# Optimization experiments

Hardware: AMD Instinct MI355X
Metric: run time of the kernel (lower is better)

The kernel has to match this reference:

```python
import jax, jax.numpy as jnp
import numpy as np

DN = ('NCHW', 'OIHW', 'NCHW')


def conv2d(x, w, b):
    y = jax.lax.conv_general_dilated(x, w, (1, 1), 'SAME', dimension_numbers=DN)
    return y + b[None, :, None, None]


def dyn_filter(x, Wa, ba, Wb, bb, Wc, bc):
    # KPN-style head: predict 81 per-pixel 9x9 filter taps, softmax-normalized.
    h = jax.nn.relu(conv2d(x, Wa, ba))
    h = jax.nn.relu(conv2d(h, Wb, bb))
    f = conv2d(h, Wc, bc)            # (N, 81, H, W)
    return jax.nn.softmax(f, axis=1)


def apply_dynamic_conv(x, f):
    # Equivalent to pad(4) + unfold(9x9) + mul + sum, without materializing
    # the (N,81,H,W)*... patch tensor: accumulate 81 shifted slices.
    N, C, H, W = x.shape  # C == 1
    xp = jnp.pad(x, ((0, 0), (0, 0), (4, 4), (4, 4)))
    out = jnp.zeros((N, 1, H, W), x.dtype)
    for dy in range(9):
        for dx in range(9):
            k = dy * 9 + dx  # matches unfold(2).unfold(3).permute(0,1,4,5,2,3) tap order
            out = out + xp[:, :, dy:dy + H, dx:dx + W] * f[:, k:k + 1]
    return out


def nearest_resize(x, oh, ow):
    _, _, ih, iw = x.shape
    ri = jnp.arange(oh) * ih // oh   # matches torch F.interpolate mode='nearest'
    rj = jnp.arange(ow) * iw // ow
    return x[:, :, ri][:, :, :, rj]


def setup_inputs() -> dict:
    key = jax.random.key(0)
    ks = jax.random.split(key, 8)
    s = 0.05
    return {
        'x': jax.random.normal(ks[0], (2, 1, 512, 512), jnp.float32),
        'g': jax.random.normal(ks[1], (2, 1, 512, 512), jnp.float32),
        'fWa': jax.random.normal(ks[2], (5, 64, 1, 3, 3), jnp.float32) * s,
        'fba': jnp.zeros((5, 64), jnp.float32),
        'fWb': jax.random.normal(ks[3], (5, 64, 64, 3, 3), jnp.float32) * s,
        'fbb': jnp.zeros((5, 64), jnp.float32),
        'fWc': jax.random.normal(ks[4], (5, 81, 64, 3, 3), jnp.float32) * s,
        'fbc': jnp.zeros((5, 81), jnp.float32),
        'W2a': jax.random.normal(ks[5], (64, 5, 3, 3), jnp.float32) * s,
        'b2a': jnp.zeros((64,), jnp.float32),
        'W2b': jax.random.normal(ks[6], (1, 64, 3, 3), jnp.float32) * s,
        'b2b': jnp.zeros((1,), jnp.float32),
    }


def reference(x, g, fWa, fba, fWb, fbb, fWc, fbc, W2a, b2a, W2b, b2b):
    N, C, h, w = x.shape
    scales = [
        x,
        nearest_resize(x, h // 2, w // 2),
        nearest_resize(x, h // 4, w // 4),
        nearest_resize(x, h // 8, w // 8),
        g,
    ]
    outs = []
    for i, s in enumerate(scales):
        f = dyn_filter(s, fWa[i], fba[i], fWb[i], fbb[i], fWc[i], fbc[i])
        y = apply_dynamic_conv(s, f)
        if y.shape[2] != h or y.shape[3] != w:
            y = nearest_resize(y, h, w)
        outs.append(y)
    cat = jnp.concatenate(outs, axis=1)  # (N, 5, h, w)
    hid = jax.nn.relu(conv2d(cat, W2a, b2a))
    return conv2d(hid, W2b, b2b)
```

## Files before the change

### kernel.cpp

```cpp
#include <hip/hip_runtime.h>
#include <math.h>

typedef _Float16 half8 __attribute__((ext_vector_type(8)));
typedef _Float16 half4v __attribute__((ext_vector_type(4)));
typedef float f32x4 __attribute__((ext_vector_type(4)));

#define LOG2E 1.44269504f

__device__ __forceinline__ void pack_generic(int rem, int NT, int COUT, float scale,
                                             const float* __restrict__ src,
                                             _Float16* __restrict__ dst) {
  int j = rem & 7, lane = (rem >> 3) & 63, rest = rem >> 9;
  int t = rest % NT, s = rest / NT;
  int oc = t * 16 + (lane & 15);
  int tap = s >> 1;
  int ic = (s & 1) * 32 + ((lane >> 4) & 3) * 8 + j;
  float v = (oc < COUT) ? src[((size_t)oc * 64 + ic) * 9 + tap] * scale : 0.f;
  dst[rem] = (_Float16)v;
}

__global__ void prep_all_kernel(const float* __restrict__ fWa, const float* __restrict__ fWb,
                                const float* __restrict__ fWc, const float* __restrict__ W2a,
                                const float* __restrict__ W2b, const float* __restrict__ x,
                                _Float16* __restrict__ Bp1, _Float16* __restrict__ BpA,
                                _Float16* __restrict__ BpB, _Float16* __restrict__ Bpb,
                                _Float16* __restrict__ Bpc,
                                _Float16* __restrict__ s1, _Float16* __restrict__ s2,
                                _Float16* __restrict__ s3) {
  int idx = blockIdx.x * blockDim.x + threadIdx.x;
  if (idx < 184320) {
    int sc = idx / 36864, rem = idx - sc * 36864;
    pack_generic(rem, 4, 64, 1.f, fWb + sc * 36864, Bpb + sc * 36864);
  } else if (idx < 460800) {
    int i2 = idx - 184320;
    int sc = i2 / 55296, rem = i2 - sc * 55296;
    pack_generic(rem, 6, 81, LOG2E, fWc + sc * 46656, Bpc + sc * 55296);
  } else if (idx < 471040) {
    int i2 = idx - 460800;
    int sc = i2 >> 11, rem = i2 & 2047;
    int j = rem & 7, lane = (rem >> 3) & 63, nt = rem >> 9;
    int oc = nt * 16 + (lane & 15);
    int k = ((lane >> 4) & 3) * 8 + j;
    float v = (k < 9) ? fWa[sc * 576 + oc * 9 + k] : 0.f;
    Bp1[sc * 2048 + rem] = (_Float16)v;
  } else if (idx < 475136) {
    int rem = idx - 471040;
    int j = rem & 7, lane = (rem >> 3) & 63;
    int nt = (rem >> 9) & 3, s = rem >> 11;
    int oc = nt * 16 + (lane & 15);
    int k = s * 32 + ((lane >> 4) & 3) * 8 + j;
    float v = 0.f;
    if (k < 45) { int ic = k / 9, tap = k - ic * 9; v = W2a[(oc * 5 + ic) * 9 + tap]; }
    BpA[rem] = (_Float16)v;
  } else if (idx < 484352) {
    pack_generic(idx - 475136, 1, 1, 1.f, W2b, BpB);
  } else if (idx < 615424) {
    int i2 = idx - 484352;
    int n = i2 >> 16, p = i2 & 65535, rr = p >> 8, cc = p & 255;
    s1[i2] = (_Float16)x[(size_t)n * 262144 + (size_t)(rr * 2) * 512 + cc * 2];
  } else if (idx < 648192) {
    int i2 = idx - 615424;
    int n = i2 >> 14, p = i2 & 16383, rr = p >> 7, cc = p & 127;
    s2[i2] = (_Float16)x[(size_t)n * 262144 + (size_t)(rr * 4) * 512 + cc * 4];
  } else if (idx < 656384) {
    int i2 = idx - 648192;
    int n = i2 >> 12, p = i2 & 4095, rr = p >> 6, cc = p & 63;
    s3[i2] = (_Float16)x[(size_t)n * 262144 + (size_t)(rr * 8) * 512 + cc * 8];
  }
}

__device__ __forceinline__ int xcd_swizzle(int bid) {
  return (bid & 7) * 596 + (bid >> 3);
}

__device__ __forceinline__ void map_block(int bid, int& sc, int& n, int& bx, int& by,
                                          int& Hs, int& RS, int& h2off) {
  if (bid < 2048) { sc = 0; Hs = 512; RS = 1; h2off = 0;
    int t = bid; n = t >> 10; t &= 1023; by = t >> 5; bx = t & 31; }
  else if (bid < 4096) { sc = 4; Hs = 512; RS = 1; h2off = 33554432;
    int t = bid - 2048; n = t >> 10; t &= 1023; by = t >> 5; bx = t & 31; }
  else if (bid < 4608) { sc = 1; Hs = 256; RS = 2; h2off = 67108864;
    int t = bid - 4096; n = t >> 8; t &= 255; by = t >> 4; bx = t & 15; }
  else if (bid < 4736) { sc = 2; Hs = 128; RS = 4; h2off = 75497472;
    int t = bid - 4608; n = t >> 6; t &= 63; by = t >> 3; bx = t & 7; }
  else { sc = 3; Hs = 64; RS = 8; h2off = 77594624;
    int t = bid - 4736; n = t >> 4; t &= 15; by = t >> 2; bx = t & 3; }
}

__device__ __forceinline__ const void* pick_src(int sc, const float* x, const float* g,
                                                const _Float16* s1, const _Float16* s2,
                                                const _Float16* s3, int& sStr, bool& f16s) {
  if (sc == 0) { sStr = 262144; f16s = false; return x; }
  if (sc == 1) { sStr = 65536; f16s = true; return s1; }
  if (sc == 2) { sStr = 16384; f16s = true; return s2; }
  if (sc == 3) { sStr = 4096; f16s = true; return s3; }
  sStr = 262144; f16s = false; return g;
}

__device__ __forceinline__ float src_load(const void* p, bool f16s, size_t off) {
  return f16s ? (float)((const _Float16*)p)[off] : ((const float*)p)[off];
}

template <int MT, int NT, bool SWAP, int NTHR>
__device__ __forceinline__ void mfma_acc18(const _Float16* slab, const half8* __restrict__ Bp,
                                           half8* __restrict__ Bs,
                                           f32x4 (&acc)[MT][NT], int tid) {
  const int lane = tid & 63;
  const int wv = tid >> 6;
  const int quad = lane >> 4;
  const int ln15 = lane & 15;
  const f32x4 zz = {0.f, 0.f, 0.f, 0.f};
#pragma unroll
  for (int mt = 0; mt < MT; ++mt)
#pragma unroll
    for (int nt = 0; nt < NT; ++nt) acc[mt][nt] = zz;
  auto step = [&](int s, half8 (&bf)[NT]) {
    const int tap = s >> 1;
    const int dy = tap / 3;
    const int dx = tap - dy * 3;
    const int C = dx + ln15;
    const int qsw = (((s & 1) * 4 + quad) ^ (C & 7));
    const _Float16* base = slab + C * 64 + qsw * 8;
    half8 af[MT];
#pragma unroll
    for (int mt = 0; mt < MT; ++mt)
      af[mt] = *(const half8*)(base + (wv * MT + mt + dy) * (18 * 64));
#pragma unroll
    for (int mt = 0; mt < MT; ++mt)
#pragma unroll
      for (int nt = 0; nt < NT; ++nt)
        acc[mt][nt] = SWAP
          ? __builtin_amdgcn_mfma_f32_16x16x32_f16(bf[nt], af[mt], acc[mt][nt], 0, 0, 0)
          : __builtin_amdgcn_mfma_f32_16x16x32_f16(af[mt], bf[nt], acc[mt][nt], 0, 0, 0);
  };
  constexpr int CH = 2 * NT * 64;
  for (int i = tid; i < CH; i += NTHR) Bs[i] = Bp[i];
  __syncthreads();
#pragma unroll 1
  for (int c = 0; c < 9; ++c) {
    const int buf = c & 1;
    if (c < 8) {
      const half8* gsrc = Bp + (2 * (c + 1)) * (NT * 64);
      half8* dst = Bs + (buf ^ 1) * CH;
      for (int i = tid; i < CH; i += NTHR) dst[i] = gsrc[i];
    }
    half8 bf[NT];
#pragma unroll
    for (int nt = 0; nt < NT; ++nt) bf[nt] = Bs[buf * CH + nt * 64 + lane];
    step(2 * c, bf);
#pragma unroll
    for (int nt = 0; nt < NT; ++nt) bf[nt] = Bs[buf * CH + NT * 64 + nt * 64 + lane];
    step(2 * c + 1, bf);
    __syncthreads();
  }
}

template <int MT, int NT, int COUT, int COUTP, bool RELU, typename OutT, int NTHR>
__device__ __forceinline__ void mfma_body(const _Float16* slab, const half8* __restrict__ Bp,
                                          half8* __restrict__ Bs,
                                          const float* __restrict__ bias,
                                          OutT* __restrict__ out,
                                          int H, int W, int gr0, int gc0, int tid) {
  f32x4 acc[MT][NT];
  mfma_acc18<MT, NT, false, NTHR>(slab, Bp, Bs, acc, tid);
  const int lane = tid & 63;
  const int wv = tid >> 6;
  const int quad = lane >> 4;
  const int ln15 = lane & 15;
  float bvv[NT];
#pragma unroll
  for (int nt = 0; nt < NT; ++nt) {
    const int oc = nt * 16 + ln15;
    bvv[nt] = (oc < COUT) ? bias[oc] : 0.f;
  }
#pragma unroll
  for (int mt = 0; mt < MT; ++mt) {
    const int gr = gr0 + wv * MT + mt;
#pragma unroll
    for (int reg = 0; reg < 4; ++reg) {
      const int gc = gc0 + quad * 4 + reg;
#pragma unroll
      for (int nt = 0; nt < NT; ++nt) {
        const int oc = nt * 16 + ln15;
        float v = acc[mt][nt][reg] + bvv[nt];
        if (RELU) v = fmaxf(v, 0.f);
        if (oc < COUTP) out[((size_t)gr * W + gc) * COUTP + oc] = (OutT)v;
      }
    }
  }
}

__global__ __launch_bounds__(512, 4)
void conv12_ms_kernel(const float* __restrict__ x, const float* __restrict__ g,
                      const _Float16* __restrict__ s1, const _Float16* __restrict__ s2,
                      const _Float16* __restrict__ s3,
                      const half8* __restrict__ Bp1b, const float* __restrict__ fba,
                      const half8* __restrict__ Bpbb, const float* __restrict__ fbb,
                      _Float16* __restrict__ h2) {
  __shared__ float xs[20 * 20];
  __shared__ __align__(16) _Float16 slab[18 * 18 * 64];
  __shared__ half8 BsS[2 * 2 * 4 * 64];
  int sc, n, bx, by, Hs, RS, h2off;
  map_block(xcd_swizzle(blockIdx.x), sc, n, bx, by, Hs, RS, h2off);
  int sStr; bool f16s;
  const void* src = pick_src(sc, x, g, s1, s2, s3, sStr, f16s);
  _Float16* out = h2 + h2off + (size_t)n * Hs * Hs * 64;
  const half8* Bp1 = Bp1b + sc * 256;
  const half8* Bp = Bpbb + sc * 4608;
  const float* ba = fba + sc * 64;
  const float* bb = fbb + sc * 64;
  const int H = Hs, W = Hs;
  const int tid = threadIdx.x;
  const int gr0 = by * 16, gc0 = bx * 16;
  for (int i = tid; i < 400; i += 512) {
    int R = i / 20, C = i % 20;
    int gr = gr0 - 2 + R, gc = gc0 - 2 + C;
    xs[i] = (gr >= 0 && gr < H && gc >= 0 && gc < W)
                ? src_load(src, f16s, (size_t)n * sStr + (size_t)gr * W + gc) : 0.f;
  }
  __syncthreads();
  const int lane = tid & 63;
  const int wv = tid >> 6;
  const int quad = lane >> 4;
  const int ln15 = lane & 15;
  half8 bf1[4];
  float b1v[4][4];
#pragma unroll
  for (int nt = 0; nt < 4; ++nt) {
    bf1[nt] = Bp1[nt * 64 + lane];
#pragma unroll
    for (int reg = 0; reg < 4; ++reg) b1v[nt][reg] = ba[nt * 16 + quad * 4 + reg];
  }
  int off1[8];
  bool v1[8];
#pragma unroll
  for (int j = 0; j < 8; ++j) {
    int k = quad * 8 + j;
    v1[j] = (k < 9);
    off1[j] = v1[j] ? ((k / 3) * 20 + (k % 3)) : 0;
  }
  const f32x4 zz = {0.f, 0.f, 0.f, 0.f};
#pragma unroll 1
  for (int mt = wv; mt < 21; mt += 8) {
    int p = mt * 16 + ln15;
    int pcl = (p < 323) ? p : 323;
    int Rg = pcl / 18, Cg = pcl - Rg * 18;
    int base = Rg * 20 + Cg;
    half8 af;
#pragma unroll
    for (int j = 0; j < 8; ++j)
      af[j] = v1[j] ? (_Float16)xs[base + off1[j]] : (_Float16)0.f;
    f32x4 a1[4] = {zz, zz, zz, zz};
#pragma unroll
    for (int nt = 0; nt < 4; ++nt)
      a1[nt] = __builtin_amdgcn_mfma_f32_16x16x32_f16(bf1[nt], af, a1[nt], 0, 0, 0);
    if (p < 324) {
      int R2 = p / 18, C2 = p - R2 * 18;
      int gr = gr0 - 1 + R2, gc = gc0 - 1 + C2;
      bool inb = (gr >= 0 && gr < H && gc >= 0 && gc < W);
      _Float16* sb = slab + p * 64 + (quad & 1) * 4;
      const int csw = C2 & 7;
#pragma unroll
      for (int nt = 0; nt < 4; ++nt) {
        half4v w;
#pragma unroll
        for (int reg = 0; reg < 4; ++reg) {
          float v = inb ? fmaxf(a1[nt][reg] + b1v[nt][reg], 0.f) : 0.f;
          w[reg] = (_Float16)v;
        }
        const int chunk = nt * 2 + (quad >> 1);
        *(half4v*)(sb + ((chunk ^ csw) * 8)) = w;
      }
    }
  }
  __syncthreads();
  mfma_body<2, 4, 64, 64, true, _Float16, 512>(slab, Bp, BsS, bb, out, H, W, gr0, gc0, tid);
}

__global__ __launch_bounds__(512, 4)
void conv3sd_ms_kernel(const _Float16* __restrict__ h2, const half8* __restrict__ Bpcb,
                       const float* __restrict__ fbc,
                       const float* __restrict__ x, const float* __restrict__ g,
                       const _Float16* __restrict__ s1, const _Float16* __restrict__ s2,
                       const _Float16* __restrict__ s3, float* __restrict__ cat) {
  constexpr int MT = 2;
  __shared__ __align__(16) _Float16 slab[324 * 40];
  __shared__ float xs[24 * 24];
  __shared__ half8 BsS[2 * 768];
  int sc, n, bx, by, Hs, RS, h2off;
  map_block(xcd_swizzle(blockIdx.x), sc, n, bx, by, Hs, RS, h2off);
  int sStr; bool f16s;
  const void* src = pick_src(sc, x, g, s1, s2, s3, sStr, f16s);
  const _Float16* in = h2 + h2off + (size_t)n * Hs * Hs * 64;
  const half8* Bp = Bpcb + sc * 6912;
  const float* bias = fbc + sc * 81;
  float* catp = cat + (size_t)(sc * 2 + n) * 262144;
  const int H = Hs, W = Hs;
  const int tid = threadIdx.x;
  const int gr0 = by * 16, gc0 = bx * 16;
  const int lane = tid & 63;
  const int wv = tid >> 6;
  const int quad = lane >> 4;
  const int ln15 = lane & 15;
  for (int i = tid; i < 576; i += 512) {
    int R = i / 24, C = i % 24;
    int gr = gr0 - 4 + R, gc = gc0 - 4 + C;
    xs[i] = (gr >= 0 && gr < H && gc >= 0 && gc < W)
                ? src_load(src, f16s, (size_t)n * sStr + (size_t)gr * W + gc) : 0.f;
  }
  auto stage_load = [&](int h, half8 (&stg)[3], int (&soff)[3], bool (&sok)[3]) {
#pragma unroll
    for (int it = 0; it < 3; ++it) {
      int i = tid + it * 512;
      bool ok = (i < 1296);
      int chunk = i & 3, px = i >> 2;
      int R = px / 18, C = px - R * 18;
      int gr = gr0 - 1 + R, gc = gc0 - 1 + C;
      half8 v = {0, 0, 0, 0, 0, 0, 0, 0};
      if (ok && gr >= 0 && gr < H && gc >= 0 && gc < W)
        v = *(const half8*)(in + ((size_t)gr * W + gc) * 64 + (h * 4 + chunk) * 8);
      stg[it] = v;
      soff[it] = px * 40 + chunk * 8;
      sok[it] = ok;
    }
  };
  auto stage_write = [&](half8 (&stg)[3], int (&soff)[3], bool (&sok)[3]) {
#pragma unroll
    for (int it = 0; it < 3; ++it)
      if (sok[it]) *(half8*)(slab + soff[it]) = stg[it];
  };
  auto stageB2 = [&](int t0, int t1, int h, int buf) {
    half8* dst = BsS + buf * 768;
    const half8* g0 = Bp + (size_t)(t0 * 2 + h) * 384;
    const half8* g1 = Bp + (size_t)(t1 * 2 + h) * 384;
#pragma unroll
    for (int it = 0; it < 2; ++it) {
      int i = tid + it * 512;
      if (i < 768) dst[i] = (i < 384) ? g0[i] : g1[i - 384];
    }
  };
  auto stageB1 = [&](int h, int buf) {
    half8* dst = BsS + buf * 768;
    const half8* g0 = Bp + (size_t)(16 + h) * 384;
    if (tid < 384) dst[tid] = g0[tid];
  };

  f32x4 acc[MT][6];
  const f32x4 zz = {0.f, 0.f, 0.f, 0.f};
#pragma unroll
  for (int mt = 0; mt < MT; ++mt)
#pragma unroll
    for (int nt = 0; nt < 6; ++nt) acc[mt][nt] = zz;

  auto ctap = [&](int tap, half8 (&bf)[6]) {
    const int dy = tap / 3;
    const int dx = tap - dy * 3;
    const int C = dx + ln15;
    const _Float16* base = slab + C * 40 + quad * 8;
    half8 af[MT];
#pragma unroll
    for (int mt = 0; mt < MT; ++mt)
      af[mt] = *(const half8*)(base + (wv * MT + mt + dy) * 720);
#pragma unroll
    for (int mt = 0; mt < MT; ++mt)
#pragma unroll
      for (int nt = 0; nt < 6; ++nt)
        acc[mt][nt] = __builtin_amdgcn_mfma_f32_16x16x32_f16(bf[nt], af[mt], acc[mt][nt], 0, 0, 0);
  };
  auto run_taps = [&](int h, int b0) {
#pragma unroll 1
    for (int c = 0; c < 4; ++c) {
      const int buf = b0 ^ (c & 1);
      if (c < 3) stageB2(2 * c + 2, 2 * c + 3, h, buf ^ 1);
      else       stageB1(h, buf ^ 1);
      half8 bf[6];
#pragma unroll
      for (int nt = 0; nt < 6; ++nt) bf[nt] = BsS[buf * 768 + nt * 64 + lane];
      ctap(2 * c, bf);
#pragma unroll
      for (int nt = 0; nt < 6; ++nt) bf[nt] = BsS[buf * 768 + 384 + nt * 64 + lane];
      ctap(2 * c + 1, bf);
      __syncthreads();
    }
    const int buf = b0;
    half8 bf[6];
#pragma unroll
    for (int nt = 0; nt < 6; ++nt) bf[nt] = BsS[buf * 768 + nt * 64 + lane];
    ctap(8, bf);
  };

  half8 stgA[3]; int soffA[3]; bool sokA[3];
  half8 stgB[3]; int soffB[3]; bool sokB[3];
  stage_load(0, stgA, soffA, sokA);
  stage_write(stgA, soffA, sokA);
  stageB2(0, 1, 0, 0);
  __syncthreads();
  stage_load(1, stgB, soffB, sokB);
  run_taps(0, 0);
  __syncthreads();
  stage_write(stgB, soffB, sokB);
  stageB2(0, 1, 1, 0);
  __syncthreads();
  run_taps(1, 0);

  float bvv[6][4];
  int dyx[6][4];
  bool vv[6][4];
#pragma unroll
  for (int nt = 0; nt < 6; ++nt)
#pragma unroll
    for (int reg = 0; reg < 4; ++reg) {
      int ch = nt * 16 + quad * 4 + reg;
      bool ok = (ch < 81);
      vv[nt][reg] = ok;
      bvv[nt][reg] = ok ? bias[ch] * LOG2E : 0.f;
      int dy = ch / 9, dx = ch - dy * 9;
      dyx[nt][reg] = ok ? dy * 24 + dx : 0;
    }
  const int lrs = (RS == 2) ? 1 : ((RS == 4) ? 2 : 3);
#pragma unroll
  for (int mt = 0; mt < MT; ++mt) {
    const float* xb = xs + (wv * MT + mt) * 24 + ln15;
    float sum = 0.f, y = 0.f;
#pragma unroll
    for (int nt = 0; nt < 6; ++nt)
#pragma unroll
      for (int reg = 0; reg < 4; ++reg) {
        if (vv[nt][reg]) {
          float e = exp2f(acc[mt][nt][reg] + bvv[nt][reg]);
          sum += e;
          y = fmaf(e, xb[dyx[nt][reg]], y);
        }
      }
    sum += __shfl_xor(sum, 16, 64);
    sum += __shfl_xor(sum, 32, 64);
    y += __shfl_xor(y, 16, 64);
    y += __shfl_xor(y, 32, 64);
    const float o = y / sum;
    const int gr = gr0 + wv * MT + mt, gc = gc0 + ln15;
    if (RS == 1) {
      if (quad == 0) catp[(size_t)gr * 512 + gc] = o;
    } else {
      for (int t = quad; t < RS * RS; t += 4) {
        int a = t >> lrs, b = t & (RS - 1);
        catp[((size_t)(gr * RS + a)) * 512 + (gc * RS + b)] = o;
      }
    }
  }
}

__global__ __launch_bounds__(512, 4)
void tail_fused_kernel(const float* __restrict__ cat,
                       const half8* __restrict__ BpA, const float* __restrict__ b2a,
                       const half8* __restrict__ BpB, const float* __restrict__ b2b,
                       float* __restrict__ out) {
  __shared__ float cs[20 * 20 * 5];
  __shared__ __align__(16) _Float16 hid[18 * 18 * 64];
  __shared__ half8 BsS[2 * 2 * 1 * 64];
  const int n = blockIdx.z;
  float* op = out + (size_t)n * (512 * 512);
  const int tid = threadIdx.x;
  const int gr0 = blockIdx.y * 16, gc0 = blockIdx.x * 16;
  for (int i = tid; i < 2000; i += 512) {
    int ic = i / 400, px = i - ic * 400;
    int R = px / 20, C = px - R * 20;
    int gr = gr0 - 2 + R, gc = gc0 - 2 + C;
    cs[px * 5 + ic] = (gr >= 0 && gr < 512 && gc >= 0 && gc < 512)
                ? cat[(size_t)(ic * 2 + n) * 262144 + (size_t)gr * 512 + gc] : 0.f;
  }
  __syncthreads();
  const int lane = tid & 63;
  const int wv = tid >> 6;
  const int quad = lane >> 4;
  const int ln15 = lane & 15;
  int goff[2][8];
  bool gok[2][8];
#pragma unroll
  for (int s = 0; s < 2; ++s)
#pragma unroll
    for (int j = 0; j < 8; ++j) {
      int k = s * 32 + quad * 8 + j;
      bool ok = (k < 45);
      int ic = k / 9;
      int tap = k - ic * 9;
      int dy = tap / 3, dx = tap - dy * 3;
      goff[s][j] = ok ? ((dy * 20 + dx) * 5 + ic) : 0;
      gok[s][j] = ok;
    }
  half8 bfA[2][4];
  float bAv[4][4];
#pragma unroll
  for (int s = 0; s < 2; ++s)
#pragma unroll
    for (int nt = 0; nt < 4; ++nt) bfA[s][nt] = BpA[(s * 4 + nt) * 64 + lane];
#pragma unroll
  for (int nt = 0; nt < 4; ++nt)
#pragma unroll
    for (int reg = 0; reg < 4; ++reg) bAv[nt][reg] = b2a[nt * 16 + quad * 4 + reg];
  const f32x4 zz = {0.f, 0.f, 0.f, 0.f};
#pragma unroll 1
  for (int mt = wv; mt < 21; mt += 8) {
    int p = mt * 16 + ln15;
    int pcl = (p < 323) ? p : 323;
    int base = (pcl / 18) * 100 + (pcl % 18) * 5;
    f32x4 acc1[4] = {zz, zz, zz, zz};
#pragma unroll
    for (int s = 0; s < 2; ++s) {
      half8 af;
#pragma unroll
      for (int j = 0; j < 8; ++j) {
        float a = gok[s][j] ? cs[base + goff[s][j]] : 0.f;
        af[j] = (_Float16)a;
      }
#pragma unroll
      for (int nt = 0; nt < 4; ++nt)
        acc1[nt] = __builtin_amdgcn_mfma_f32_16x16x32_f16(bfA[s][nt], af, acc1[nt], 0, 0, 0);
    }
    if (p < 324) {
      int R2 = p / 18, C2 = p - R2 * 18;
      int gr = gr0 - 1 + R2, gc = gc0 - 1 + C2;
      bool inb = (gr >= 0 && gr < 512 && gc >= 0 && gc < 512);
      _Float16* sb = hid + p * 64 + (quad & 1) * 4;
      const int csw = C2 & 7;
#pragma unroll
      for (int nt = 0; nt < 4; ++nt) {
        half4v w;
#pragma unroll
        for (int reg = 0; reg < 4; ++reg) {
          float v = inb ? fmaxf(acc1[nt][reg] + bAv[nt][reg], 0.f) : 0.f;
          w[reg] = (_Float16)v;
        }
        const int chunk = nt * 2 + (quad >> 1);
        *(half4v*)(sb + ((chunk ^ csw) * 8)) = w;
      }
    }
  }
  __syncthreads();
  mfma_body<2, 1, 1, 1, false, float, 512>(hid, BpB, BsS, b2b, op, 512, 512, gr0, gc0, tid);
}

extern "C" void kernel_launch(void* const* d_in, const int* in_sizes, int n_in,
                              void* d_out, int out_size, void* d_ws, size_t ws_size,
                              hipStream_t stream) {
  (void)in_sizes; (void)n_in; (void)out_size; (void)ws_size;
  const float* x   = (const float*)d_in[0];
  const float* g   = (const float*)d_in[1];
  const float* fWa = (const float*)d_in[2];
  const float* fba = (const float*)d_in[3];
  const float* fWb = (const float*)d_in[4];
  const float* fbb = (const float*)d_in[5];
  const float* fWc = (const float*)d_in[6];
  const float* fbc = (const float*)d_in[7];
  const float* W2a = (const float*)d_in[8];
  const float* b2a = (const float*)d_in[9];
  const float* W2b = (const float*)d_in[10];
  const float* b2b = (const float*)d_in[11];
  float* out = (float*)d_out;
  float* ws = (float*)d_ws;

  float* Bp1F = ws;
  float* BpAF = Bp1F + 5120;
  float* BpBF = BpAF + 2048;
  float* BpbF = BpBF + 4608;
  float* BpcF = BpbF + 92160;
  float* s1F  = BpcF + 138240;
  float* s2F  = s1F + 65536;
  float* s3F  = s2F + 16384;
  float* cat  = s3F + 4096;
  float* h2F  = cat + 2621440;
  _Float16* s1 = (_Float16*)s1F;
  _Float16* s2 = (_Float16*)s2F;
  _Float16* s3 = (_Float16*)s3F;
  _Float16* h2 = (_Float16*)h2F;
  const half8* Bp1 = (const half8*)Bp1F;
  const half8* BpA = (const half8*)BpAF;
  const half8* BpB = (const half8*)BpBF;
  const half8* Bpb = (const half8*)BpbF;
  const half8* Bpc = (const half8*)BpcF;

  prep_all_kernel<<<2564, 256, 0, stream>>>(fWa, fWb, fWc, W2a, W2b, x,
                                            (_Float16*)Bp1F, (_Float16*)BpAF,
                                            (_Float16*)BpBF, (_Float16*)BpbF,
                                            (_Float16*)BpcF, s1, s2, s3);
  conv12_ms_kernel<<<4768, 512, 0, stream>>>(x, g, s1, s2, s3, Bp1, fba, Bpb, fbb, h2);
  conv3sd_ms_kernel<<<4768, 512, 0, stream>>>(h2, Bpc, fbc, x, g, s1, s2, s3, cat);
  tail_fused_kernel<<<dim3(32, 32, 2), 512, 0, stream>>>(cat, BpA, b2a, BpB, b2b, out);
}
```

Baseline: 377.4 us.

## Enlarge conv3 tile to 32x16 pixels and drop register-staged slab prefetch

The fused conv3/softmax/dynamic-conv kernel now gives each block a 32x16 output tile (MT=4) instead of 16x16, halving the grid and adding new block-mapping and XCD swizzle helpers. This amortizes the per-block weight staging and the halo loads over more pixels. The register-staged prefetch of the second input half is replaced with direct global-to-LDS staging after the first half's compute. The trade-off is more LDS and registers per block, launch bounds lowered to 2 blocks per SM, and less overlap of loads with MFMA work.

After: 427.7 us. +13.3%, slower.

```diff
diff --git a/kernel.cpp b/kernel.cpp
--- a/kernel.cpp
+++ b/kernel.cpp
@@ -87,6 +87,24 @@
     int t = bid - 4736; n = t >> 4; t &= 15; by = t >> 2; bx = t & 3; }
 }
 
+__device__ __forceinline__ int xcd_swizzle32(int bid) {
+  return (bid & 7) * 298 + (bid >> 3);
+}
+
+__device__ __forceinline__ void map_block32(int bid, int& sc, int& n, int& bx, int& by,
+                                            int& Hs, int& RS, int& h2off) {
+  if (bid < 1024) { sc = 0; Hs = 512; RS = 1; h2off = 0;
+    int t = bid; n = t >> 9; t &= 511; by = t >> 5; bx = t & 31; }
+  else if (bid < 2048) { sc = 4; Hs = 512; RS = 1; h2off = 33554432;
+    int t = bid - 1024; n = t >> 9; t &= 511; by = t >> 5; bx = t & 31; }
+  else if (bid < 2304) { sc = 1; Hs = 256; RS = 2; h2off = 67108864;
+    int t = bid - 2048; n = t >> 7; t &= 127; by = t >> 4; bx = t & 15; }
+  else if (bid < 2368) { sc = 2; Hs = 128; RS = 4; h2off = 75497472;
+    int t = bid - 2304; n = t >> 5; t &= 31; by = t >> 3; bx = t & 7; }
+  else { sc = 3; Hs = 64; RS = 8; h2off = 77594624;
+    int t = bid - 2368; n = t >> 3; t &= 7; by = t >> 2; bx = t & 3; }
+}
+
 __device__ __forceinline__ const void* pick_src(int sc, const float* x, const float* g,
                                                 const _Float16* s1, const _Float16* s2,
                                                 const _Float16* s3, int& sStr, bool& f16s) {
@@ -277,18 +295,18 @@
   mfma_body<2, 4, 64, 64, true, _Float16, 512>(slab, Bp, BsS, bb, out, H, W, gr0, gc0, tid);
 }
 
-__global__ __launch_bounds__(512, 4)
+__global__ __launch_bounds__(512, 2)
 void conv3sd_ms_kernel(const _Float16* __restrict__ h2, const half8* __restrict__ Bpcb,
                        const float* __restrict__ fbc,
                        const float* __restrict__ x, const float* __restrict__ g,
                        const _Float16* __restrict__ s1, const _Float16* __restrict__ s2,
                        const _Float16* __restrict__ s3, float* __restrict__ cat) {
-  constexpr int MT = 2;
-  __shared__ __align__(16) _Float16 slab[324 * 40];
-  __shared__ float xs[24 * 24];
+  constexpr int MT = 4;
+  __shared__ __align__(16) _Float16 slab[612 * 40];
+  __shared__ float xs[40 * 24];
   __shared__ half8 BsS[2 * 768];
   int sc, n, bx, by, Hs, RS, h2off;
-  map_block(xcd_swizzle(blockIdx.x), sc, n, bx, by, Hs, RS, h2off);
+  map_block32(xcd_swizzle32(blockIdx.x), sc, n, bx, by, Hs, RS, h2off);
   int sStr; bool f16s;
   const void* src = pick_src(sc, x, g, s1, s2, s3, sStr, f16s);
   const _Float16* in = h2 + h2off + (size_t)n * Hs * Hs * 64;
@@ -297,37 +315,28 @@
   float* catp = cat + (size_t)(sc * 2 + n) * 262144;
   const int H = Hs, W = Hs;
   const int tid = threadIdx.x;
-  const int gr0 = by * 16, gc0 = bx * 16;
+  const int gr0 = by * 32, gc0 = bx * 16;
   const int lane = tid & 63;
   const int wv = tid >> 6;
   const int quad = lane >> 4;
   const int ln15 = lane & 15;
-  for (int i = tid; i < 576; i += 512) {
+  for (int i = tid; i < 960; i += 512) {
     int R = i / 24, C = i % 24;
     int gr = gr0 - 4 + R, gc = gc0 - 4 + C;
     xs[i] = (gr >= 0 && gr < H && gc >= 0 && gc < W)
                 ? src_load(src, f16s, (size_t)n * sStr + (size_t)gr * W + gc) : 0.f;
   }
-  auto stage_load = [&](int h, half8 (&stg)[3], int (&soff)[3], bool (&sok)[3]) {
-#pragma unroll
-    for (int it = 0; it < 3; ++it) {
-      int i = tid + it * 512;
-      bool ok = (i < 1296);
+  auto stage_slab = [&](int h) {
+#pragma unroll 1
+    for (int i = tid; i < 2448; i += 512) {
       int chunk = i & 3, px = i >> 2;
       int R = px / 18, C = px - R * 18;
       int gr = gr0 - 1 + R, gc = gc0 - 1 + C;
       half8 v = {0, 0, 0, 0, 0, 0, 0, 0};
-      if (ok && gr >= 0 && gr < H && gc >= 0 && gc < W)
+      if (gr >= 0 && gr < H && gc >= 0 && gc < W)
         v = *(const half8*)(in + ((size_t)gr * W + gc) * 64 + (h * 4 + chunk) * 8);
-      stg[it] = v;
-      soff[it] = px * 40 + chunk * 8;
-      sok[it] = ok;
-    }
-  };
-  auto stage_write = [&](half8 (&stg)[3], int (&soff)[3], bool (&sok)[3]) {
-#pragma unroll
-    for (int it = 0; it < 3; ++it)
-      if (sok[it]) *(half8*)(slab + soff[it]) = stg[it];
+      *(half8*)(slab + px * 40 + chunk * 8) = v;
+    }
   };
   auto stageB2 = [&](int t0, int t1, int h, int buf) {
     half8* dst = BsS + buf * 768;
@@ -389,16 +398,12 @@
     ctap(8, bf);
   };
 
-  half8 stgA[3]; int soffA[3]; bool sokA[3];
-  half8 stgB[3]; int soffB[3]; bool sokB[3];
-  stage_load(0, stgA, soffA, sokA);
-  stage_write(stgA, soffA, sokA);
+  stage_slab(0);
   stageB2(0, 1, 0, 0);
   __syncthreads();
-  stage_load(1, stgB, soffB, sokB);
   run_taps(0, 0);
   __syncthreads();
-  stage_write(stgB, soffB, sokB);
+  stage_slab(1);
   stageB2(0, 1, 1, 0);
   __syncthreads();
   run_taps(1, 0);
@@ -583,6 +588,6 @@
                                             (_Float16*)BpBF, (_Float16*)BpbF,
                                             (_Float16*)BpcF, s1, s2, s3);
   conv12_ms_kernel<<<4768, 512, 0, stream>>>(x, g, s1, s2, s3, Bp1, fba, Bpb, fbb, h2);
-  conv3sd_ms_kernel<<<4768, 512, 0, stream>>>(h2, Bpc, fbc, x, g, s1, s2, s3, cat);
+  conv3sd_ms_kernel<<<2384, 512, 0, stream>>>(h2, Bpc, fbc, x, g, s1, s2, s3, cat);
   tail_fused_kernel<<<dim3(32, 32, 2), 512, 0, stream>>>(cat, BpA, b2a, BpB, b2b, out);
 }
```

## Load conv3 input slab and weights via global_load_lds with XOR swizzle

Applied to the files above, without the earlier changes.

Restructures the final 64->81 conv stage. The full 64-channel halo slab now goes into LDS in a single pass, using direct global-to-LDS loads for interior tiles and an XOR-swizzled layout, instead of two 32-channel halves staged through registers. Weights are double-buffered per tap using 4-byte direct-to-LDS loads with vmcnt/barrier pipelining, and s_setprio is raised around the MFMA blocks. The larger LDS footprint lowers the occupancy target from 4 to 2 blocks per CU.

New measurement: 383.9 us. About the same (+1.7%).

```diff
diff --git a/kernel.cpp b/kernel.cpp
--- a/kernel.cpp
+++ b/kernel.cpp
@@ -6,6 +6,16 @@
 typedef float f32x4 __attribute__((ext_vector_type(4)));
 
 #define LOG2E 1.44269504f
+
+typedef __attribute__((address_space(1))) const unsigned int gas_u32;
+typedef __attribute__((address_space(3))) unsigned int las_u32;
+
+__device__ __forceinline__ void gll16(const void* gsrc, void* ldst) {
+  __builtin_amdgcn_global_load_lds((gas_u32*)gsrc, (las_u32*)ldst, 16, 0, 0);
+}
+__device__ __forceinline__ void gll4(const void* gsrc, void* ldst) {
+  __builtin_amdgcn_global_load_lds((gas_u32*)gsrc, (las_u32*)ldst, 4, 0, 0);
+}
 
 __device__ __forceinline__ void pack_generic(int rem, int NT, int COUT, float scale,
                                              const float* __restrict__ src,
@@ -277,16 +287,15 @@
   mfma_body<2, 4, 64, 64, true, _Float16, 512>(slab, Bp, BsS, bb, out, H, W, gr0, gc0, tid);
 }
 
-__global__ __launch_bounds__(512, 4)
+__global__ __launch_bounds__(512, 2)
 void conv3sd_ms_kernel(const _Float16* __restrict__ h2, const half8* __restrict__ Bpcb,
                        const float* __restrict__ fbc,
                        const float* __restrict__ x, const float* __restrict__ g,
                        const _Float16* __restrict__ s1, const _Float16* __restrict__ s2,
                        const _Float16* __restrict__ s3, float* __restrict__ cat) {
-  constexpr int MT = 2;
-  __shared__ __align__(16) _Float16 slab[324 * 40];
+  __shared__ __align__(16) _Float16 slab[384 * 64];
+  __shared__ __align__(16) _Float16 Bsd[2][6144];
   __shared__ float xs[24 * 24];
-  __shared__ half8 BsS[2 * 768];
   int sc, n, bx, by, Hs, RS, h2off;
   map_block(xcd_swizzle(blockIdx.x), sc, n, bx, by, Hs, RS, h2off);
   int sStr; bool f16s;
@@ -302,106 +311,100 @@
   const int wv = tid >> 6;
   const int quad = lane >> 4;
   const int ln15 = lane & 15;
+
   for (int i = tid; i < 576; i += 512) {
     int R = i / 24, C = i % 24;
     int gr = gr0 - 4 + R, gc = gc0 - 4 + C;
     xs[i] = (gr >= 0 && gr < H && gc >= 0 && gc < W)
                 ? src_load(src, f16s, (size_t)n * sStr + (size_t)gr * W + gc) : 0.f;
   }
-  auto stage_load = [&](int h, half8 (&stg)[3], int (&soff)[3], bool (&sok)[3]) {
-#pragma unroll
-    for (int it = 0; it < 3; ++it) {
-      int i = tid + it * 512;
-      bool ok = (i < 1296);
-      int chunk = i & 3, px = i >> 2;
+
+  const bool interior = (gr0 > 0) && (gc0 > 0) && (gr0 + 17 <= H) && (gc0 + 17 <= W);
+  if (interior) {
+    const int pxb0 = wv * 48;
+#pragma unroll
+    for (int k = 0; k < 6; ++k) {
+      const int pxb = pxb0 + k * 8;
+      int px = pxb + (lane >> 3);
+      int pcl = (px < 324) ? px : 323;
+      int R = pcl / 18, C = pcl - R * 18;
+      int l = (lane & 7) ^ (C & 7);
+      gll16((const char*)(in + ((size_t)(gr0 - 1 + R) * W + (gc0 - 1 + C)) * 64 + l * 8),
+            (char*)slab + (size_t)pxb * 128);
+    }
+  } else {
+    for (int i = tid; i < 2592; i += 512) {
+      int px = i >> 3, pslot = i & 7;
       int R = px / 18, C = px - R * 18;
       int gr = gr0 - 1 + R, gc = gc0 - 1 + C;
+      int l = pslot ^ (C & 7);
       half8 v = {0, 0, 0, 0, 0, 0, 0, 0};
-      if (ok && gr >= 0 && gr < H && gc >= 0 && gc < W)
-        v = *(const half8*)(in + ((size_t)gr * W + gc) * 64 + (h * 4 + chunk) * 8);
-      stg[it] = v;
-      soff[it] = px * 40 + chunk * 8;
-      sok[it] = ok;
-    }
+      if (gr >= 0 && gr < H && gc >= 0 && gc < W)
+        v = *(const half8*)(in + ((size_t)gr * W + gc) * 64 + l * 8);
+      *(half8*)(slab + (size_t)px * 64 + pslot * 8) = v;
+    }
+  }
+
+  auto stageB = [&](int t, int buf) {
+    const char* s = (const char*)(Bp + (size_t)t * 768) + wv * 1536 + lane * 4;
+    char* d = (char*)(&Bsd[buf][0]) + wv * 1536;
+#pragma unroll
+    for (int i = 0; i < 6; ++i) gll4(s + i * 256, d + i * 256);
   };
-  auto stage_write = [&](half8 (&stg)[3], int (&soff)[3], bool (&sok)[3]) {
-#pragma unroll
-    for (int it = 0; it < 3; ++it)
-      if (sok[it]) *(half8*)(slab + soff[it]) = stg[it];
+  stageB(0, 0);
+  stageB(1, 1);
+  asm volatile("s_waitcnt lgkmcnt(0)" ::: "memory");
+
+  f32x4 acc[2][6];
+  const f32x4 zz = {0.f, 0.f, 0.f, 0.f};
+#pragma unroll
+  for (int mt = 0; mt < 2; ++mt)
+#pragma unroll
+    for (int nt = 0; nt < 6; ++nt) acc[mt][nt] = zz;
+
+  auto tap_body = [&](int t, int buf) {
+    const int dy = t / 3, dx = t - dy * 3;
+    const int C = dx + ln15;
+    const int cx = C & 7;
+    const _Float16* bb = &Bsd[buf][0];
+#pragma unroll
+    for (int h = 0; h < 2; ++h) {
+      half8 bf[6];
+#pragma unroll
+      for (int nt = 0; nt < 6; ++nt)
+        bf[nt] = *(const half8*)(bb + h * 3072 + (nt * 64 + lane) * 8);
+      half8 af[2];
+#pragma unroll
+      for (int mt = 0; mt < 2; ++mt) {
+        const int px = (wv * 2 + mt + dy) * 18 + C;
+        af[mt] = *(const half8*)(slab + (size_t)px * 64 + ((h * 4 + quad) ^ cx) * 8);
+      }
+      __builtin_amdgcn_s_setprio(1);
+#pragma unroll
+      for (int mt = 0; mt < 2; ++mt)
+#pragma unroll
+        for (int nt = 0; nt < 6; ++nt)
+          acc[mt][nt] =
+              __builtin_amdgcn_mfma_f32_16x16x32_f16(bf[nt], af[mt], acc[mt][nt], 0, 0, 0);
+      __builtin_amdgcn_s_setprio(0);
+    }
   };
-  auto stageB2 = [&](int t0, int t1, int h, int buf) {
-    half8* dst = BsS + buf * 768;
-    const half8* g0 = Bp + (size_t)(t0 * 2 + h) * 384;
-    const half8* g1 = Bp + (size_t)(t1 * 2 + h) * 384;
-#pragma unroll
-    for (int it = 0; it < 2; ++it) {
-      int i = tid + it * 512;
-      if (i < 768) dst[i] = (i < 384) ? g0[i] : g1[i - 384];
-    }
-  };
-  auto stageB1 = [&](int h, int buf) {
-    half8* dst = BsS + buf * 768;
-    const half8* g0 = Bp + (size_t)(16 + h) * 384;
-    if (tid < 384) dst[tid] = g0[tid];
-  };
-
-  f32x4 acc[MT][6];
-  const f32x4 zz = {0.f, 0.f, 0.f, 0.f};
-#pragma unroll
-  for (int mt = 0; mt < MT; ++mt)
-#pragma unroll
-    for (int nt = 0; nt < 6; ++nt) acc[mt][nt] = zz;
-
-  auto ctap = [&](int tap, half8 (&bf)[6]) {
-    const int dy = tap / 3;
-    const int dx = tap - dy * 3;
-    const int C = dx + ln15;
-    const _Float16* base = slab + C * 40 + quad * 8;
-    half8 af[MT];
-#pragma unroll
-    for (int mt = 0; mt < MT; ++mt)
-      af[mt] = *(const half8*)(base + (wv * MT + mt + dy) * 720);
-#pragma unroll
-    for (int mt = 0; mt < MT; ++mt)
-#pragma unroll
-      for (int nt = 0; nt < 6; ++nt)
-        acc[mt][nt] = __builtin_amdgcn_mfma_f32_16x16x32_f16(bf[nt], af[mt], acc[mt][nt], 0, 0, 0);
-  };
-  auto run_taps = [&](int h, int b0) {
+
 #pragma unroll 1
-    for (int c = 0; c < 4; ++c) {
-      const int buf = b0 ^ (c & 1);
-      if (c < 3) stageB2(2 * c + 2, 2 * c + 3, h, buf ^ 1);
-      else       stageB1(h, buf ^ 1);
-      half8 bf[6];
-#pragma unroll
-      for (int nt = 0; nt < 6; ++nt) bf[nt] = BsS[buf * 768 + nt * 64 + lane];
-      ctap(2 * c, bf);
-#pragma unroll
-      for (int nt = 0; nt < 6; ++nt) bf[nt] = BsS[buf * 768 + 384 + nt * 64 + lane];
-      ctap(2 * c + 1, bf);
-      __syncthreads();
-    }
-    const int buf = b0;
-    half8 bf[6];
-#pragma unroll
-    for (int nt = 0; nt < 6; ++nt) bf[nt] = BsS[buf * 768 + nt * 64 + lane];
-    ctap(8, bf);
-  };
-
-  half8 stgA[3]; int soffA[3]; bool sokA[3];
-  half8 stgB[3]; int soffB[3]; bool sokB[3];
-  stage_load(0, stgA, soffA, sokA);
-  stage_write(stgA, soffA, sokA);
-  stageB2(0, 1, 0, 0);
-  __syncthreads();
-  stage_load(1, stgB, soffB, sokB);
-  run_taps(0, 0);
-  __syncthreads();
-  stage_write(stgB, soffB, sokB);
-  stageB2(0, 1, 1, 0);
-  __syncthreads();
-  run_taps(1, 0);
+  for (int t = 0; t < 8; ++t) {
+    if (t >= 1) stageB(t + 1, (t + 1) & 1);
+    asm volatile("s_waitcnt vmcnt(6)" ::: "memory");
+    __builtin_amdgcn_s_barrier();
+    asm volatile("" ::: "memory");
+    tap_body(t, t & 1);
+    asm volatile("s_waitcnt lgkmcnt(0)" ::: "memory");
+    __builtin_amdgcn_s_barrier();
+    asm volatile("" ::: "memory");
+  }
+  asm volatile("s_waitcnt vmcnt(0)" ::: "memory");
+  __builtin_amdgcn_s_barrier();
+  asm volatile("" ::: "memory");
+  tap_body(8, 0);
 
   float bvv[6][4];
   int dyx[6][4];
@@ -419,8 +422,8 @@
     }
   const int lrs = (RS == 2) ? 1 : ((RS == 4) ? 2 : 3);
 #pragma unroll
-  for (int mt = 0; mt < MT; ++mt) {
-    const float* xb = xs + (wv * MT + mt) * 24 + ln15;
+  for (int mt = 0; mt < 2; ++mt) {
+    const float* xb = xs + (wv * 2 + mt) * 24 + ln15;
     float sum = 0.f, y = 0.f;
 #pragma unroll
     for (int nt = 0; nt < 6; ++nt)
@@ -437,7 +440,7 @@
     y += __shfl_xor(y, 16, 64);
     y += __shfl_xor(y, 32, 64);
     const float o = y / sum;
-    const int gr = gr0 + wv * MT + mt, gc = gc0 + ln15;
+    const int gr = gr0 + wv * 2 + mt, gc = gc0 + ln15;
     if (RS == 1) {
       if (quad == 0) catp[(size_t)gr * 512 + gc] = o;
     } else {
```
